# Kernel optimization log

Measured on AMD Instinct MI355X. Metric: run time of the kernel, lower is better.

## Reference

```python
import jax, jax.numpy as jnp
import numpy as np

N_NODES = 100000
N_EDGES = 3200000
N_GRAPHS = 512
D_IN = 128
N_CLASSES = 10
BN_EPS = 1e-5


def gcn_conv(x, W, b, src, dst, n_nodes):
    """PyG GCNConv: symmetric-normalized mean aggregation with self-loops."""
    h = x @ W  # [N, F_out]
    ones = jnp.ones(src.shape[0], h.dtype)
    deg = jax.ops.segment_sum(ones, dst, num_segments=n_nodes) + 1.0  # +1 self-loop
    dinv = jax.lax.rsqrt(deg)
    norm = dinv[src] * dinv[dst]  # [E]
    agg = jax.ops.segment_sum(h[src] * norm[:, None], dst, num_segments=n_nodes)
    agg = agg + h * (dinv * dinv)[:, None]  # self-loop contribution
    return agg + b


def bn_relu_lin(x, W, b, gamma, beta):
    """One MLP block: Linear -> ReLU -> BatchNorm1d (training-mode stats)."""
    h = jax.nn.relu(x @ W + b)
    m = h.mean(axis=0)
    v = h.var(axis=0)  # biased, like torch BN
    return gamma * (h - m) * jax.lax.rsqrt(v + BN_EPS) + beta


def setup_inputs() -> dict:
    key = jax.random.key(0)
    ks = jax.random.split(key, 16)
    x = jax.random.normal(ks[0], (N_NODES, D_IN), dtype=jnp.float32)
    edge_index = jax.random.randint(ks[1], (2, N_EDGES), 0, N_NODES, dtype=jnp.int64)
    batch = jnp.sort(jax.random.randint(ks[2], (N_NODES,), 0, N_GRAPHS, dtype=jnp.int64))

    def lin(k, fi, fo):
        s = 1.0 / np.sqrt(fi)
        kw, kb = jax.random.split(k)
        return (jax.random.uniform(kw, (fi, fo), jnp.float32, -s, s),
                jax.random.uniform(kb, (fo,), jnp.float32, -s, s))

    W1, b1 = lin(ks[3], D_IN, 32)
    W2, b2 = lin(ks[4], 32, 64)
    lin1_W, lin1_b = lin(ks[5], 96, 96)
    m1_W, m1_b = lin(ks[6], 96, 96)
    m2_W, m2_b = lin(ks[7], 96, N_CLASSES)
    return dict(
        x=x, edge_index=edge_index, batch=batch,
        W1=W1, b1=b1, W2=W2, b2=b2,
        lin1_W=lin1_W, lin1_b=lin1_b,
        lin1_g=jnp.ones((96,), jnp.float32), lin1_bt=jnp.zeros((96,), jnp.float32),
        m1_W=m1_W, m1_b=m1_b,
        m1_g=jnp.ones((96,), jnp.float32), m1_bt=jnp.zeros((96,), jnp.float32),
        m2_W=m2_W, m2_b=m2_b,
        m2_g=jnp.ones((N_CLASSES,), jnp.float32), m2_bt=jnp.zeros((N_CLASSES,), jnp.float32),
    )


def reference(x, edge_index, batch, W1, b1, W2, b2, lin1_W, lin1_b, lin1_g, lin1_bt,
              m1_W, m1_b, m1_g, m1_bt, m2_W, m2_b, m2_g, m2_bt):
    src, dst = edge_index[0], edge_index[1]
    x1 = gcn_conv(x, W1, b1, src, dst, N_NODES)   # [N, 32]
    x2 = gcn_conv(x1, W2, b2, src, dst, N_NODES)  # [N, 64]
    h = jnp.concatenate([x1, x2], axis=1)          # [N, 96]
    h = bn_relu_lin(h, lin1_W, lin1_b, lin1_g, lin1_bt)
    # global max pool over graphs
    pooled = jax.ops.segment_max(h, batch, num_segments=N_GRAPHS)
    pooled = jnp.where(jnp.isfinite(pooled), pooled, 0.0)  # guard empty segments
    h = bn_relu_lin(pooled, m1_W, m1_b, m1_g, m1_bt)
    out = bn_relu_lin(h, m2_W, m2_b, m2_g, m2_bt)  # [G, C]
    return out
```

## Files before the change

### kernel.cpp

```cpp
#include <hip/hip_runtime.h>
#include <hip/hip_fp16.h>

#define NN 100000
#define NE 3200000
#define NG 512
#define DIN 128
#define F1 32
#define F2 64
#define FC 96
#define NC 10
#define BNEPS 1e-5f

#define BSH 8
#define NBUK 391
#define EPB 16384
#define NBLK 196
#define SCAN_N (NBUK * NBLK)
#define SCAN_NB ((SCAN_N + 1023) / 1024)

typedef unsigned int uint;

__device__ __forceinline__ void atomAddF(float* p, float v) { unsafeAtomicAdd(p, v); }
__device__ __forceinline__ float2 h2f(uint u) {
  __half2 h = *reinterpret_cast<__half2*>(&u);
  return __half22float2(h);
}
__device__ __forceinline__ uint f2h2(float a, float b) {
  __half2 h = __floats2half2_rn(a, b);
  return *reinterpret_cast<uint*>(&h);
}

__global__ __launch_bounds__(256) void k_hist(const int* __restrict__ dst,
                                              unsigned* __restrict__ bhist) {
  __shared__ unsigned h[NBUK];
  int t = threadIdx.x, b = blockIdx.x;
  for (int i = t; i < NBUK; i += 256) h[i] = 0;
  __syncthreads();
  int beg = b * EPB, end = min(beg + EPB, NE);
  for (int e = beg + t; e < end; e += 256) atomicAdd(&h[dst[e] >> BSH], 1u);
  __syncthreads();
  for (int i = t; i < NBUK; i += 256) bhist[(size_t)i * NBLK + b] = h[i];
}

__global__ __launch_bounds__(256) void k_scan1(unsigned* __restrict__ data, int n,
                                               unsigned* __restrict__ bsum) {
  __shared__ unsigned ts[256];
  int b = blockIdx.x, t = threadIdx.x;
  int base = b * 1024 + t * 4;
  unsigned v0 = 0, v1 = 0, v2 = 0, v3 = 0;
  if (base + 3 < n) {
    uint4 u = *(const uint4*)&data[base];
    v0 = u.x; v1 = u.y; v2 = u.z; v3 = u.w;
  } else {
    if (base < n) v0 = data[base];
    if (base + 1 < n) v1 = data[base + 1];
    if (base + 2 < n) v2 = data[base + 2];
    if (base + 3 < n) v3 = data[base + 3];
  }
  unsigned s = v0 + v1 + v2 + v3;
  ts[t] = s;
  __syncthreads();
  for (int d = 1; d < 256; d <<= 1) {
    unsigned add = (t >= d) ? ts[t - d] : 0u;
    __syncthreads();
    ts[t] += add;
    __syncthreads();
  }
  unsigned run = ts[t] - s;
  if (t == 255) bsum[b] = ts[255];
  if (base < n) data[base] = run;
  run += v0;
  if (base + 1 < n) data[base + 1] = run;
  run += v1;
  if (base + 2 < n) data[base + 2] = run;
  run += v2;
  if (base + 3 < n) data[base + 3] = run;
}

__global__ void k_scan2(unsigned* __restrict__ bsum, int nb) {
  __shared__ unsigned ts[512];
  int t = threadIdx.x;
  unsigned v = (t < nb) ? bsum[t] : 0u;
  ts[t] = v;
  __syncthreads();
  for (int d = 1; d < 512; d <<= 1) {
    unsigned a = (t >= d) ? ts[t - d] : 0u;
    __syncthreads();
    ts[t] += a;
    __syncthreads();
  }
  if (t < nb) bsum[t] = ts[t] - v;
}

__global__ void k_scan3(unsigned* __restrict__ data, int n, const unsigned* __restrict__ bsum,
                        int total) {
  int i = blockIdx.x * 256 + threadIdx.x;
  if (i < n) data[i] += bsum[i >> 10];
  if (i == 0) data[n] = (unsigned)total;
}

__global__ __launch_bounds__(256) void k_binwrite(const int* __restrict__ src,
                                                  const int* __restrict__ dst,
                                                  const unsigned* __restrict__ offs2,
                                                  int* __restrict__ packed) {
  __shared__ unsigned cur[NBUK];
  int t = threadIdx.x, b = blockIdx.x;
  for (int i = t; i < NBUK; i += 256) cur[i] = offs2[(size_t)i * NBLK + b];
  __syncthreads();
  int beg = b * EPB, end = min(beg + EPB, NE);
  for (int e = beg + t; e < end; e += 256) {
    int d = dst[e];
    unsigned pos = atomicAdd(&cur[d >> BSH], 1u);
    packed[pos] = (src[e] << BSH) | (d & 255);
  }
}

__global__ __launch_bounds__(256) void k_bsort(const int* __restrict__ packed,
                                               const unsigned* __restrict__ offs2,
                                               int* __restrict__ csr,
                                               int* __restrict__ offs,
                                               float* __restrict__ dinv) {
  int buk = blockIdx.x, t = threadIdx.x;
  __shared__ unsigned cnt[256];
  __shared__ int cur[256];
  __shared__ unsigned wsum[4];
  cnt[t] = 0;
  __syncthreads();
  unsigned beg = offs2[(size_t)buk * NBLK], end = offs2[(size_t)(buk + 1) * NBLK];
  for (unsigned j = beg + t; j < end; j += 256) atomicAdd(&cnt[packed[j] & 255], 1u);
  __syncthreads();
  unsigned v = cnt[t];
  unsigned inc = v;
#pragma unroll
  for (int d = 1; d < 64; d <<= 1) {
    unsigned o = __shfl_up(inc, d, 64);
    if ((t & 63) >= d) inc += o;
  }
  int wv = t >> 6;
  if ((t & 63) == 63) wsum[wv] = inc;
  __syncthreads();
  unsigned woff = 0;
  for (int i = 0; i < wv; ++i) woff += wsum[i];
  unsigned ex = woff + inc - v;
  cur[t] = (int)(beg + ex);
  int node = (buk << BSH) + t;
  if (node < NN) {
    offs[node] = (int)(beg + ex);
    dinv[node] = rsqrtf((float)v + 1.0f);
  } else if (node == NN) {
    offs[NN] = (int)(beg + ex);
  }
  __syncthreads();
  for (unsigned j = beg + t; j < end; j += 256) {
    int p = packed[j];
    int pos = atomicAdd(&cur[p & 255], 1);
    csr[pos] = p >> BSH;
  }
}

__global__ void k_gbound(const int* __restrict__ batch, int* __restrict__ gstart) {
  int i = blockIdx.x * 256 + threadIdx.x;
  if (i >= NN) return;
  int b = batch[i], p = i ? batch[i - 1] : -1;
  for (int g = p + 1; g <= b; ++g) gstart[g] = i;
  if (i == NN - 1)
    for (int g = b + 1; g <= NG; ++g) gstart[g] = NN;
}

__global__ __launch_bounds__(256) void k_gemm1(const float* __restrict__ x,
                                               const float* __restrict__ W,
                                               const float* __restrict__ dinv,
                                               __half* __restrict__ h1sh) {
  __shared__ __align__(16) float Ws[DIN * F1];
  __shared__ __align__(16) float xs[64][DIN + 4];
  int t = threadIdx.x;
  for (int i = t; i < DIN * F1 / 4; i += 256)
    *(float4*)&Ws[i * 4] = *(const float4*)&W[i * 4];
  int row0 = blockIdx.x * 64;
  for (int i = t; i < 64 * 32; i += 256) {
    int r = i >> 5, q = i & 31;
    int row = row0 + r;
    float4 v = (row < NN) ? *(const float4*)&x[(size_t)row * DIN + q * 4]
                          : make_float4(0.f, 0.f, 0.f, 0.f);
    *(float4*)&xs[r][q * 4] = v;
  }
  __syncthreads();
  int cg = t & 7, rg = t >> 3;
  int c0 = cg * 4, r0 = rg * 2;
  float acc[2][4];
#pragma unroll
  for (int i = 0; i < 2; ++i)
#pragma unroll
    for (int j = 0; j < 4; ++j) acc[i][j] = 0.f;
#pragma unroll 4
  for (int k = 0; k < DIN; k += 4) {
    float4 xv0 = *(float4*)&xs[r0][k];
    float4 xv1 = *(float4*)&xs[r0 + 1][k];
    float4 wf[4];
#pragma unroll
    for (int m = 0; m < 4; ++m) wf[m] = *(float4*)&Ws[(k + m) * F1 + c0];
    const float* x0 = (const float*)&xv0;
    const float* x1 = (const float*)&xv1;
#pragma unroll
    for (int m = 0; m < 4; ++m) {
      const float* wp = (const float*)&wf[m];
#pragma unroll
      for (int j = 0; j < 4; ++j) {
        acc[0][j] += x0[m] * wp[j];
        acc[1][j] += x1[m] * wp[j];
      }
    }
  }
#pragma unroll
  for (int i = 0; i < 2; ++i) {
    int row = row0 + r0 + i;
    if (row < NN) {
      float dv = dinv[row];
      uint2 o;
      o.x = f2h2(acc[i][0] * dv, acc[i][1] * dv);
      o.y = f2h2(acc[i][2] * dv, acc[i][3] * dv);
      *(uint2*)&h1sh[(size_t)row * F1 + c0] = o;
    }
  }
}

__global__ __launch_bounds__(256) void k_gather1(const ushort* __restrict__ hs,
                                                 const int* __restrict__ offs,
                                                 const int* __restrict__ csr,
                                                 const float* __restrict__ dinv,
                                                 const float* __restrict__ bias,
                                                 float* __restrict__ out1,
                                                 uint* __restrict__ out2) {
  int node = blockIdx.x * 4 + (threadIdx.x >> 6);
  int lane = threadIdx.x & 63;
  int slot = lane >> 3, f4 = (lane & 7) * 4;
  int beg = offs[node], end = offs[node + 1];
  float ax = 0.f, ay = 0.f, az = 0.f, aw = 0.f;
  int j = beg + slot;
  for (; j + 8 < end; j += 16) {
    int s0 = csr[j], s1 = csr[j + 8];
    uint2 u0 = *(const uint2*)&hs[(size_t)s0 * F1 + f4];
    uint2 u1 = *(const uint2*)&hs[(size_t)s1 * F1 + f4];
    float2 a0 = h2f(u0.x), b0 = h2f(u0.y), a1 = h2f(u1.x), b1 = h2f(u1.y);
    ax += a0.x + a1.x; ay += a0.y + a1.y;
    az += b0.x + b1.x; aw += b0.y + b1.y;
  }
  if (j < end) {
    int s0 = csr[j];
    uint2 u0 = *(const uint2*)&hs[(size_t)s0 * F1 + f4];
    float2 a0 = h2f(u0.x), b0 = h2f(u0.y);
    ax += a0.x; ay += a0.y; az += b0.x; aw += b0.y;
  }
#pragma unroll
  for (int m = 8; m < 64; m <<= 1) {
    ax += __shfl_xor(ax, m, 64); ay += __shfl_xor(ay, m, 64);
    az += __shfl_xor(az, m, 64); aw += __shfl_xor(aw, m, 64);
  }
  if (slot == 0) {
    float dv = dinv[node];
    uint2 su = *(const uint2*)&hs[(size_t)node * F1 + f4];
    float2 sa = h2f(su.x), sb = h2f(su.y);
    float4 bb = *(const float4*)&bias[f4];
    float vx = dv * (sa.x + ax) + bb.x;
    float vy = dv * (sa.y + ay) + bb.y;
    float vz = dv * (sb.x + az) + bb.z;
    float vw = dv * (sb.y + aw) + bb.w;
    *(float4*)&out1[(size_t)node * FC + f4] = make_float4(vx, vy, vz, vw);
    uint2 o;
    o.x = f2h2(vx * dv, vy * dv);
    o.y = f2h2(vz * dv, vw * dv);
    *(uint2*)&out2[(size_t)node * 16 + (f4 >> 1)] = o;
  }
}

__global__ __launch_bounds__(256) void k_gather2f(const ushort* __restrict__ hs,
                                                  const int* __restrict__ offs,
                                                  const int* __restrict__ csr,
                                                  const float* __restrict__ dinv,
                                                  const float* __restrict__ W2,
                                                  const float* __restrict__ b2,
                                                  float* __restrict__ hcat) {
  __shared__ float rowbuf[4][F1];
  int wv = threadIdx.x >> 6;
  int node = blockIdx.x * 4 + wv;
  int lane = threadIdx.x & 63;
  int slot = lane >> 3, f4 = (lane & 7) * 4;
  int beg = offs[node], end = offs[node + 1];
  float ax = 0.f, ay = 0.f, az = 0.f, aw = 0.f;
  int j = beg + slot;
  for (; j + 8 < end; j += 16) {
    int s0 = csr[j], s1 = csr[j + 8];
    uint2 u0 = *(const uint2*)&hs[(size_t)s0 * F1 + f4];
    uint2 u1 = *(const uint2*)&hs[(size_t)s1 * F1 + f4];
    float2 a0 = h2f(u0.x), b0 = h2f(u0.y), a1 = h2f(u1.x), b1 = h2f(u1.y);
    ax += a0.x + a1.x; ay += a0.y + a1.y;
    az += b0.x + b1.x; aw += b0.y + b1.y;
  }
  if (j < end) {
    int s0 = csr[j];
    uint2 u0 = *(const uint2*)&hs[(size_t)s0 * F1 + f4];
    float2 a0 = h2f(u0.x), b0 = h2f(u0.y);
    ax += a0.x; ay += a0.y; az += b0.x; aw += b0.y;
  }
#pragma unroll
  for (int m = 8; m < 64; m <<= 1) {
    ax += __shfl_xor(ax, m, 64); ay += __shfl_xor(ay, m, 64);
    az += __shfl_xor(az, m, 64); aw += __shfl_xor(aw, m, 64);
  }
  if (slot == 0) {
    float dv = dinv[node];
    uint2 su = *(const uint2*)&hs[(size_t)node * F1 + f4];
    float2 sa = h2f(su.x), sb = h2f(su.y);
    *(float4*)&rowbuf[wv][f4] = make_float4(
        dv * (sa.x + ax), dv * (sa.y + ay),
        dv * (sb.x + az), dv * (sb.y + aw));
  }
  __syncthreads();
  const float* row = rowbuf[wv];
  float acc = b2[lane];
#pragma unroll
  for (int k = 0; k < F1; ++k) acc += row[k] * W2[k * F2 + lane];
  hcat[(size_t)node * FC + F1 + lane] = acc;
}

__global__ __launch_bounds__(384) void k_lin1(const float* __restrict__ hcat,
                                              const float* __restrict__ W,
                                              const float* __restrict__ b,
                                              float* __restrict__ y,
                                              float* __restrict__ colsum,
                                              float* __restrict__ colsumsq) {
  __shared__ __align__(16) float lds[16000];
  float* sW = lds;
  float* sX = lds + 9600;
  int t = threadIdx.x;
  for (int i = t; i < 96 * 24; i += 384) {
    int k = i / 24, c0 = (i % 24) * 4;
    float4 v = *(const float4*)&W[i * 4];
    *(float4*)&sW[k * 100 + c0] = v;
  }
  int row0 = blockIdx.x * 64;
  for (int i = t; i < 64 * 24; i += 384) {
    int r = i / 24, q = (i % 24) * 4;
    int row = row0 + r;
    float4 v = (row < NN) ? *(const float4*)&hcat[(size_t)row * FC + q]
                          : make_float4(0.f, 0.f, 0.f, 0.f);
    *(float4*)&sX[r * 100 + q] = v;
  }
  __syncthreads();
  int tx = t % 24, ty = t / 24;
  int c0 = tx * 4, r0 = ty * 4;
  float acc[4][4];
#pragma unroll
  for (int i = 0; i < 4; ++i)
#pragma unroll
    for (int j = 0; j < 4; ++j) acc[i][j] = 0.f;
#pragma unroll 4
  for (int k0 = 0; k0 < 96; k0 += 4) {
    float4 xf[4], wf[4];
#pragma unroll
    for (int i = 0; i < 4; ++i) xf[i] = *(float4*)&sX[(r0 + i) * 100 + k0];
#pragma unroll
    for (int m = 0; m < 4; ++m) wf[m] = *(float4*)&sW[(k0 + m) * 100 + c0];
#pragma unroll
    for (int i = 0; i < 4; ++i) {
      const float* xp = (const float*)&xf[i];
#pragma unroll
      for (int m = 0; m < 4; ++m) {
        const float* wp = (const float*)&wf[m];
#pragma unroll
        for (int j = 0; j < 4; ++j) acc[i][j] += xp[m] * wp[j];
      }
    }
  }
  float4 bb = *(const float4*)&b[c0];
  const float* bp = (const float*)&bb;
  float colp[4] = {0.f, 0.f, 0.f, 0.f}, colq[4] = {0.f, 0.f, 0.f, 0.f};
#pragma unroll
  for (int i = 0; i < 4; ++i) {
    int row = row0 + r0 + i;
    if (row < NN) {
      float v0 = fmaxf(acc[i][0] + bp[0], 0.f);
      float v1 = fmaxf(acc[i][1] + bp[1], 0.f);
      float v2 = fmaxf(acc[i][2] + bp[2], 0.f);
      float v3 = fmaxf(acc[i][3] + bp[3], 0.f);
      *(float4*)&y[(size_t)row * FC + c0] = make_float4(v0, v1, v2, v3);
      colp[0] += v0; colp[1] += v1; colp[2] += v2; colp[3] += v3;
      colq[0] += v0 * v0; colq[1] += v1 * v1; colq[2] += v2 * v2; colq[3] += v3 * v3;
    }
  }
  __syncthreads();
  float* ps = sX;
  float* pq = sX + 1536;
  *(float4*)&ps[ty * 96 + c0] = make_float4(colp[0], colp[1], colp[2], colp[3]);
  *(float4*)&pq[ty * 96 + c0] = make_float4(colq[0], colq[1], colq[2], colq[3]);
  __syncthreads();
  if (t < 96) {
    float s = 0.f, s2 = 0.f;
#pragma unroll
    for (int i = 0; i < 16; ++i) { s += ps[i * 96 + t]; s2 += pq[i * 96 + t]; }
    atomAddF(&colsum[t], s);
    atomAddF(&colsumsq[t], s2);
  }
}

__global__ __launch_bounds__(768) void k_pool(const float* __restrict__ y,
                                              const int* __restrict__ gstart,
                                              float* __restrict__ pooled) {
  int g = blockIdx.x, t = threadIdx.x;
  int c = t % FC, h = t / FC;
  int beg = gstart[g], end = gstart[g + 1];
  float m0 = 0.f, m1 = 0.f;
  int r = beg + h;
  for (; r + 8 < end; r += 16) {
    m0 = fmaxf(m0, y[(size_t)r * FC + c]);
    m1 = fmaxf(m1, y[(size_t)(r + 8) * FC + c]);
  }
  if (r < end) m0 = fmaxf(m0, y[(size_t)r * FC + c]);
  m0 = fmaxf(m0, m1);
  __shared__ float sh[8][FC];
  sh[h][c] = m0;
  __syncthreads();
  if (h == 0) {
    float m = sh[0][c];
#pragma unroll
    for (int i = 1; i < 8; ++i) m = fmaxf(m, sh[i][c]);
    pooled[(size_t)g * FC + c] = (end > beg) ? m : 0.f;
  }
}

__global__ void k_poolbn(const float* __restrict__ pooled, const float* __restrict__ colsum,
                         const float* __restrict__ colsumsq, const int* __restrict__ gstart,
                         const float* __restrict__ g1, const float* __restrict__ bt1,
                         float* __restrict__ pbn) {
  int idx = blockIdx.x * 256 + threadIdx.x;
  if (idx < NG * FC) {
    int g = idx / FC, c = idx % FC;
    float m = colsum[c] * (1.f / NN);
    float var = colsumsq[c] * (1.f / NN) - m * m;
    float rs = rsqrtf(var + BNEPS);
    float v = (gstart[g + 1] > gstart[g]) ? (g1[c] * (pooled[idx] - m) * rs + bt1[c]) : 0.f;
    pbn[idx] = v;
  }
}

__global__ __launch_bounds__(256) void k_mlp(const float* __restrict__ X, int ncol,
                                             const float* __restrict__ W,
                                             const float* __restrict__ b,
                                             const float* __restrict__ g,
                                             const float* __restrict__ bt,
                                             float* __restrict__ out) {
  int c = blockIdx.x, t = threadIdx.x;
  __shared__ float vals[NG];
  __shared__ float red[256], redq[256];
  __shared__ float wc[FC];
  if (t < FC) wc[t] = W[(size_t)t * ncol + c];
  __syncthreads();
  float psum = 0.f, psq = 0.f;
  for (int r = t; r < NG; r += 256) {
    float acc = b[c];
#pragma unroll
    for (int k = 0; k < FC; ++k) acc += X[(size_t)r * FC + k] * wc[k];
    float v = fmaxf(acc, 0.f);
    vals[r] = v;
    psum += v;
    psq += v * v;
  }
  red[t] = psum;
  redq[t] = psq;
  __syncthreads();
  for (int s = 128; s > 0; s >>= 1) {
    if (t < s) { red[t] += red[t + s]; redq[t] += redq[t + s]; }
    __syncthreads();
  }
  float m = red[0] * (1.f / NG);
  float var = redq[0] * (1.f / NG) - m * m;
  float rs = rsqrtf(var + BNEPS);
  float gg = g[c], bb = bt[c];
  for (int r = t; r < NG; r += 256) out[(size_t)r * ncol + c] = gg * (vals[r] - m) * rs + bb;
}

extern "C" void kernel_launch(void* const* d_in, const int* in_sizes, int n_in,
                              void* d_out, int out_size, void* d_ws, size_t ws_size,
                              hipStream_t stream) {
  const float* x    = (const float*)d_in[0];
  const int* ei     = (const int*)d_in[1];
  const int* src    = ei;
  const int* dst    = ei + NE;
  const int* batch  = (const int*)d_in[2];
  const float* W1   = (const float*)d_in[3];
  const float* b1   = (const float*)d_in[4];
  const float* W2   = (const float*)d_in[5];
  const float* b2   = (const float*)d_in[6];
  const float* l1W  = (const float*)d_in[7];
  const float* l1b  = (const float*)d_in[8];
  const float* l1g  = (const float*)d_in[9];
  const float* l1bt = (const float*)d_in[10];
  const float* m1W  = (const float*)d_in[11];
  const float* m1b  = (const float*)d_in[12];
  const float* m1g  = (const float*)d_in[13];
  const float* m1bt = (const float*)d_in[14];
  const float* m2W  = (const float*)d_in[15];
  const float* m2b  = (const float*)d_in[16];
  const float* m2g  = (const float*)d_in[17];
  const float* m2bt = (const float*)d_in[18];
  float* out = (float*)d_out;

  float* ws = (float*)d_ws;
  const size_t o_csum   = 0;
  const size_t o_csq    = 128;
  const size_t o_dinv   = 256;
  const size_t o_gstart = 100608;
  const size_t o_offs   = 101128;
  const size_t o_offs2  = 201488;
  const size_t o_bsum   = 507840;
  const size_t o_packed = 508144;
  const size_t o_h1sh   = 3708144;
  const size_t o_x1sh   = 5308144;
  const size_t o_csr    = 6908144;
  const size_t o_hcat   = 10108144;

  float* csum     = ws + o_csum;
  float* csq      = ws + o_csq;
  float* dinv     = ws + o_dinv;
  int* gstart     = (int*)(ws + o_gstart);
  int* offs       = (int*)(ws + o_offs);
  unsigned* offs2 = (unsigned*)(ws + o_offs2);
  unsigned* bsum  = (unsigned*)(ws + o_bsum);
  int* packed     = (int*)(ws + o_packed);
  __half* h1sh    = (__half*)(ws + o_h1sh);
  uint* x1sh      = (uint*)(ws + o_x1sh);
  int* csr        = (int*)(ws + o_csr);
  float* hcat     = ws + o_hcat;
  float* y        = ws + o_packed;
  float* pooled   = ws + o_offs2;
  float* pbn      = ws + o_offs2 + 49152;
  float* h3       = ws + o_offs2 + 98304;

  hipMemsetAsync(ws, 0, 256 * sizeof(float), stream);

  k_hist<<<NBLK, 256, 0, stream>>>(dst, offs2);
  k_scan1<<<SCAN_NB, 256, 0, stream>>>(offs2, SCAN_N, bsum);
  k_scan2<<<1, 512, 0, stream>>>(bsum, SCAN_NB);
  k_scan3<<<(SCAN_N + 255) / 256, 256, 0, stream>>>(offs2, SCAN_N, bsum, NE);
  k_binwrite<<<NBLK, 256, 0, stream>>>(src, dst, offs2, packed);
  k_bsort<<<NBUK, 256, 0, stream>>>(packed, offs2, csr, offs, dinv);
  k_gbound<<<(NN + 255) / 256, 256, 0, stream>>>(batch, gstart);

  k_gemm1<<<(NN + 63) / 64, 256, 0, stream>>>(x, W1, dinv, h1sh);
  k_gather1<<<NN / 4, 256, 0, stream>>>((const ushort*)h1sh, offs, csr, dinv, b1, hcat, x1sh);
  k_gather2f<<<NN / 4, 256, 0, stream>>>((const ushort*)x1sh, offs, csr, dinv, W2, b2, hcat);

  k_lin1<<<(NN + 63) / 64, 384, 0, stream>>>(hcat, l1W, l1b, y, csum, csq);
  k_pool<<<NG, 768, 0, stream>>>(y, gstart, pooled);
  k_poolbn<<<(NG * FC + 255) / 256, 256, 0, stream>>>(pooled, csum, csq, gstart, l1g, l1bt, pbn);

  k_mlp<<<FC, 256, 0, stream>>>(pbn, FC, m1W, m1b, m1g, m1bt, h3);
  k_mlp<<<NC, 256, 0, stream>>>(h3, NC, m2W, m2b, m2g, m2bt, out);
}
```

Measured before the change: 339.8 us.

## Split fp16 feature tables into 16-column halves for cache-resident gathers

Splits the 32-wide fp16 node feature tables into two 16-column arrays and runs each gather pass over one half, so each random-access table is half the size and more likely to stay in L2/MALL. The first-layer aggregation becomes two passes, and the second becomes a half-pass into a temp buffer plus a fused pass that combines both halves before the 32x64 projection. This adds two extra passes over the CSR indices and extra launches in exchange for better locality on the gathered feature rows.

```diff
diff --git a/kernel.cpp b/kernel.cpp
--- a/kernel.cpp
+++ b/kernel.cpp
@@ -170,7 +170,8 @@
 __global__ __launch_bounds__(256) void k_gemm1(const float* __restrict__ x,
                                                const float* __restrict__ W,
                                                const float* __restrict__ dinv,
-                                               __half* __restrict__ h1sh) {
+                                               ushort* __restrict__ h1a,
+                                               ushort* __restrict__ h1b) {
   __shared__ __align__(16) float Ws[DIN * F1];
   __shared__ __align__(16) float xs[64][DIN + 4];
   int t = threadIdx.x;
@@ -211,6 +212,8 @@
       }
     }
   }
+  ushort* dst = (c0 < 16) ? h1a : h1b;
+  int cc = c0 & 15;
 #pragma unroll
   for (int i = 0; i < 2; ++i) {
     int row = row0 + r0 + i;
@@ -219,61 +222,66 @@
       uint2 o;
       o.x = f2h2(acc[i][0] * dv, acc[i][1] * dv);
       o.y = f2h2(acc[i][2] * dv, acc[i][3] * dv);
-      *(uint2*)&h1sh[(size_t)row * F1 + c0] = o;
+      *(uint2*)&dst[(size_t)row * 16 + cc] = o;
     }
   }
 }
 
-__global__ __launch_bounds__(256) void k_gather1(const ushort* __restrict__ hs,
-                                                 const int* __restrict__ offs,
-                                                 const int* __restrict__ csr,
-                                                 const float* __restrict__ dinv,
-                                                 const float* __restrict__ bias,
-                                                 float* __restrict__ out1,
-                                                 uint* __restrict__ out2) {
+__global__ __launch_bounds__(256) void k_ghalf(const ushort* __restrict__ hs,
+                                               const int* __restrict__ offs,
+                                               const int* __restrict__ csr,
+                                               const float* __restrict__ dinv,
+                                               const float* __restrict__ bias,
+                                               float* __restrict__ out1,
+                                               uint* __restrict__ out2, int scale2) {
   int node = blockIdx.x * 4 + (threadIdx.x >> 6);
   int lane = threadIdx.x & 63;
-  int slot = lane >> 3, f4 = (lane & 7) * 4;
+  int slot = lane >> 2, fq = (lane & 3) * 4;
   int beg = offs[node], end = offs[node + 1];
   float ax = 0.f, ay = 0.f, az = 0.f, aw = 0.f;
   int j = beg + slot;
-  for (; j + 8 < end; j += 16) {
-    int s0 = csr[j], s1 = csr[j + 8];
-    uint2 u0 = *(const uint2*)&hs[(size_t)s0 * F1 + f4];
-    uint2 u1 = *(const uint2*)&hs[(size_t)s1 * F1 + f4];
+  for (; j + 16 < end; j += 32) {
+    int s0 = csr[j], s1 = csr[j + 16];
+    uint2 u0 = *(const uint2*)&hs[(size_t)s0 * 16 + fq];
+    uint2 u1 = *(const uint2*)&hs[(size_t)s1 * 16 + fq];
     float2 a0 = h2f(u0.x), b0 = h2f(u0.y), a1 = h2f(u1.x), b1 = h2f(u1.y);
     ax += a0.x + a1.x; ay += a0.y + a1.y;
     az += b0.x + b1.x; aw += b0.y + b1.y;
   }
   if (j < end) {
     int s0 = csr[j];
-    uint2 u0 = *(const uint2*)&hs[(size_t)s0 * F1 + f4];
+    uint2 u0 = *(const uint2*)&hs[(size_t)s0 * 16 + fq];
     float2 a0 = h2f(u0.x), b0 = h2f(u0.y);
     ax += a0.x; ay += a0.y; az += b0.x; aw += b0.y;
   }
 #pragma unroll
-  for (int m = 8; m < 64; m <<= 1) {
+  for (int m = 4; m < 64; m <<= 1) {
     ax += __shfl_xor(ax, m, 64); ay += __shfl_xor(ay, m, 64);
     az += __shfl_xor(az, m, 64); aw += __shfl_xor(aw, m, 64);
   }
   if (slot == 0) {
     float dv = dinv[node];
-    uint2 su = *(const uint2*)&hs[(size_t)node * F1 + f4];
+    uint2 su = *(const uint2*)&hs[(size_t)node * 16 + fq];
     float2 sa = h2f(su.x), sb = h2f(su.y);
-    float4 bb = *(const float4*)&bias[f4];
-    float vx = dv * (sa.x + ax) + bb.x;
-    float vy = dv * (sa.y + ay) + bb.y;
-    float vz = dv * (sb.x + az) + bb.z;
-    float vw = dv * (sb.y + aw) + bb.w;
-    *(float4*)&out1[(size_t)node * FC + f4] = make_float4(vx, vy, vz, vw);
-    uint2 o;
-    o.x = f2h2(vx * dv, vy * dv);
-    o.y = f2h2(vz * dv, vw * dv);
-    *(uint2*)&out2[(size_t)node * 16 + (f4 >> 1)] = o;
-  }
-}
-
-__global__ __launch_bounds__(256) void k_gather2f(const ushort* __restrict__ hs,
+    float vx = dv * (sa.x + ax), vy = dv * (sa.y + ay);
+    float vz = dv * (sb.x + az), vw = dv * (sb.y + aw);
+    if (bias) {
+      float4 bb = *(const float4*)&bias[fq];
+      vx += bb.x; vy += bb.y; vz += bb.z; vw += bb.w;
+    }
+    if (out1) *(float4*)&out1[(size_t)node * FC + fq] = make_float4(vx, vy, vz, vw);
+    if (out2) {
+      float s = scale2 ? dv : 1.f;
+      uint2 o;
+      o.x = f2h2(vx * s, vy * s);
+      o.y = f2h2(vz * s, vw * s);
+      *(uint2*)&out2[(size_t)node * 8 + (fq >> 1)] = o;
+    }
+  }
+}
+
+__global__ __launch_bounds__(256) void k_gather2b(const ushort* __restrict__ hs,
+                                                  const ushort* __restrict__ tmplo,
                                                   const int* __restrict__ offs,
                                                   const int* __restrict__ csr,
                                                   const float* __restrict__ dinv,
@@ -284,36 +292,43 @@
   int wv = threadIdx.x >> 6;
   int node = blockIdx.x * 4 + wv;
   int lane = threadIdx.x & 63;
-  int slot = lane >> 3, f4 = (lane & 7) * 4;
+  int slot = lane >> 2, fq = (lane & 3) * 4;
   int beg = offs[node], end = offs[node + 1];
   float ax = 0.f, ay = 0.f, az = 0.f, aw = 0.f;
   int j = beg + slot;
-  for (; j + 8 < end; j += 16) {
-    int s0 = csr[j], s1 = csr[j + 8];
-    uint2 u0 = *(const uint2*)&hs[(size_t)s0 * F1 + f4];
-    uint2 u1 = *(const uint2*)&hs[(size_t)s1 * F1 + f4];
+  for (; j + 16 < end; j += 32) {
+    int s0 = csr[j], s1 = csr[j + 16];
+    uint2 u0 = *(const uint2*)&hs[(size_t)s0 * 16 + fq];
+    uint2 u1 = *(const uint2*)&hs[(size_t)s1 * 16 + fq];
     float2 a0 = h2f(u0.x), b0 = h2f(u0.y), a1 = h2f(u1.x), b1 = h2f(u1.y);
     ax += a0.x + a1.x; ay += a0.y + a1.y;
     az += b0.x + b1.x; aw += b0.y + b1.y;
   }
   if (j < end) {
     int s0 = csr[j];
-    uint2 u0 = *(const uint2*)&hs[(size_t)s0 * F1 + f4];
+    uint2 u0 = *(const uint2*)&hs[(size_t)s0 * 16 + fq];
     float2 a0 = h2f(u0.x), b0 = h2f(u0.y);
     ax += a0.x; ay += a0.y; az += b0.x; aw += b0.y;
   }
 #pragma unroll
-  for (int m = 8; m < 64; m <<= 1) {
+  for (int m = 4; m < 64; m <<= 1) {
     ax += __shfl_xor(ax, m, 64); ay += __shfl_xor(ay, m, 64);
     az += __shfl_xor(az, m, 64); aw += __shfl_xor(aw, m, 64);
   }
   if (slot == 0) {
     float dv = dinv[node];
-    uint2 su = *(const uint2*)&hs[(size_t)node * F1 + f4];
+    uint2 su = *(const uint2*)&hs[(size_t)node * 16 + fq];
     float2 sa = h2f(su.x), sb = h2f(su.y);
-    *(float4*)&rowbuf[wv][f4] = make_float4(
-        dv * (sa.x + ax), dv * (sa.y + ay),
-        dv * (sb.x + az), dv * (sb.y + aw));
+    rowbuf[wv][16 + fq + 0] = dv * (sa.x + ax);
+    rowbuf[wv][16 + fq + 1] = dv * (sa.y + ay);
+    rowbuf[wv][16 + fq + 2] = dv * (sb.x + az);
+    rowbuf[wv][16 + fq + 3] = dv * (sb.y + aw);
+    uint2 tl = *(const uint2*)&tmplo[(size_t)node * 16 + fq];
+    float2 ta = h2f(tl.x), tb = h2f(tl.y);
+    rowbuf[wv][fq + 0] = ta.x;
+    rowbuf[wv][fq + 1] = ta.y;
+    rowbuf[wv][fq + 2] = tb.x;
+    rowbuf[wv][fq + 3] = tb.y;
   }
   __syncthreads();
   const float* row = rowbuf[wv];
@@ -514,8 +529,10 @@
   const size_t o_offs2  = 201488;
   const size_t o_bsum   = 507840;
   const size_t o_packed = 508144;
-  const size_t o_h1sh   = 3708144;
-  const size_t o_x1sh   = 5308144;
+  const size_t o_h1a    = 3708144;
+  const size_t o_h1b    = 4508144;
+  const size_t o_x1a    = 5308144;
+  const size_t o_x1b    = 6108144;
   const size_t o_csr    = 6908144;
   const size_t o_hcat   = 10108144;
 
@@ -527,8 +544,11 @@
   unsigned* offs2 = (unsigned*)(ws + o_offs2);
   unsigned* bsum  = (unsigned*)(ws + o_bsum);
   int* packed     = (int*)(ws + o_packed);
-  __half* h1sh    = (__half*)(ws + o_h1sh);
-  uint* x1sh      = (uint*)(ws + o_x1sh);
+  ushort* h1a     = (ushort*)(ws + o_h1a);
+  ushort* h1b     = (ushort*)(ws + o_h1b);
+  ushort* x1a     = (ushort*)(ws + o_x1a);
+  ushort* x1b     = (ushort*)(ws + o_x1b);
+  ushort* a2tmp   = (ushort*)(ws + o_h1a);
   int* csr        = (int*)(ws + o_csr);
   float* hcat     = ws + o_hcat;
   float* y        = ws + o_packed;
@@ -546,9 +566,12 @@
   k_bsort<<<NBUK, 256, 0, stream>>>(packed, offs2, csr, offs, dinv);
   k_gbound<<<(NN + 255) / 256, 256, 0, stream>>>(batch, gstart);
 
-  k_gemm1<<<(NN + 63) / 64, 256, 0, stream>>>(x, W1, dinv, h1sh);
-  k_gather1<<<NN / 4, 256, 0, stream>>>((const ushort*)h1sh, offs, csr, dinv, b1, hcat, x1sh);
-  k_gather2f<<<NN / 4, 256, 0, stream>>>((const ushort*)x1sh, offs, csr, dinv, W2, b2, hcat);
+  k_gemm1<<<(NN + 63) / 64, 256, 0, stream>>>(x, W1, dinv, h1a, h1b);
+  k_ghalf<<<NN / 4, 256, 0, stream>>>(h1a, offs, csr, dinv, b1, hcat, (uint*)x1a, 1);
+  k_ghalf<<<NN / 4, 256, 0, stream>>>(h1b, offs, csr, dinv, b1 + 16, hcat + 16, (uint*)x1b, 1);
+  k_ghalf<<<NN / 4, 256, 0, stream>>>(x1a, offs, csr, dinv, (const float*)nullptr,
+                                      (float*)nullptr, (uint*)a2tmp, 0);
+  k_gather2b<<<NN / 4, 256, 0, stream>>>(x1b, a2tmp, offs, csr, dinv, W2, b2, hcat);
 
   k_lin1<<<(NN + 63) / 64, 384, 0, stream>>>(hcat, l1W, l1b, y, csum, csq);
   k_pool<<<NG, 768, 0, stream>>>(y, gstart, pooled);
```

After: 396.8 us. +16.8%, slower.

## Fuse global max pooling into lin1 epilogue via integer atomicMax

Applied to the files above, without the earlier changes.

The separate pooling kernel, which re-read the full post-ReLU activation matrix, is removed. lin1 now stages each tile's ReLU outputs in shared memory and does a segmented max over the block's rows using per-row graph ids. Each segment is flushed with an integer atomicMax on the float bits, which is valid because the values are non-negative. This saves writing and re-reading a 100000x96 float intermediate and one launch, at the cost of a larger memset to zero the pooled buffer and a serial 64-row scan in 96 threads per block.

```diff
diff --git a/kernel.cpp b/kernel.cpp
--- a/kernel.cpp
+++ b/kernel.cpp
@@ -326,10 +326,12 @@
 __global__ __launch_bounds__(384) void k_lin1(const float* __restrict__ hcat,
                                               const float* __restrict__ W,
                                               const float* __restrict__ b,
-                                              float* __restrict__ y,
+                                              const int* __restrict__ batch,
+                                              float* __restrict__ pooled,
                                               float* __restrict__ colsum,
                                               float* __restrict__ colsumsq) {
   __shared__ __align__(16) float lds[16000];
+  __shared__ int bts[64];
   float* sW = lds;
   float* sX = lds + 9600;
   int t = threadIdx.x;
@@ -346,6 +348,7 @@
                           : make_float4(0.f, 0.f, 0.f, 0.f);
     *(float4*)&sX[r * 100 + q] = v;
   }
+  if (t < 64) bts[t] = (row0 + t < NN) ? batch[row0 + t] : -1;
   __syncthreads();
   int tx = t % 24, ty = t / 24;
   int c0 = tx * 4, r0 = ty * 4;
@@ -375,6 +378,7 @@
   float4 bb = *(const float4*)&b[c0];
   const float* bp = (const float*)&bb;
   float colp[4] = {0.f, 0.f, 0.f, 0.f}, colq[4] = {0.f, 0.f, 0.f, 0.f};
+  float yv[4][4];
 #pragma unroll
   for (int i = 0; i < 4; ++i) {
     int row = row0 + r0 + i;
@@ -383,14 +387,19 @@
       float v1 = fmaxf(acc[i][1] + bp[1], 0.f);
       float v2 = fmaxf(acc[i][2] + bp[2], 0.f);
       float v3 = fmaxf(acc[i][3] + bp[3], 0.f);
-      *(float4*)&y[(size_t)row * FC + c0] = make_float4(v0, v1, v2, v3);
+      yv[i][0] = v0; yv[i][1] = v1; yv[i][2] = v2; yv[i][3] = v3;
       colp[0] += v0; colp[1] += v1; colp[2] += v2; colp[3] += v3;
       colq[0] += v0 * v0; colq[1] += v1 * v1; colq[2] += v2 * v2; colq[3] += v3 * v3;
+    } else {
+      yv[i][0] = yv[i][1] = yv[i][2] = yv[i][3] = 0.f;
     }
   }
   __syncthreads();
-  float* ps = sX;
-  float* pq = sX + 1536;
+#pragma unroll
+  for (int i = 0; i < 4; ++i)
+    *(float4*)&sX[(r0 + i) * 100 + c0] = make_float4(yv[i][0], yv[i][1], yv[i][2], yv[i][3]);
+  float* ps = sW;
+  float* pq = sW + 1536;
   *(float4*)&ps[ty * 96 + c0] = make_float4(colp[0], colp[1], colp[2], colp[3]);
   *(float4*)&pq[ty * 96 + c0] = make_float4(colq[0], colq[1], colq[2], colq[3]);
   __syncthreads();
@@ -400,31 +409,18 @@
     for (int i = 0; i < 16; ++i) { s += ps[i * 96 + t]; s2 += pq[i * 96 + t]; }
     atomAddF(&colsum[t], s);
     atomAddF(&colsumsq[t], s2);
-  }
-}
-
-__global__ __launch_bounds__(768) void k_pool(const float* __restrict__ y,
-                                              const int* __restrict__ gstart,
-                                              float* __restrict__ pooled) {
-  int g = blockIdx.x, t = threadIdx.x;
-  int c = t % FC, h = t / FC;
-  int beg = gstart[g], end = gstart[g + 1];
-  float m0 = 0.f, m1 = 0.f;
-  int r = beg + h;
-  for (; r + 8 < end; r += 16) {
-    m0 = fmaxf(m0, y[(size_t)r * FC + c]);
-    m1 = fmaxf(m1, y[(size_t)(r + 8) * FC + c]);
-  }
-  if (r < end) m0 = fmaxf(m0, y[(size_t)r * FC + c]);
-  m0 = fmaxf(m0, m1);
-  __shared__ float sh[8][FC];
-  sh[h][c] = m0;
-  __syncthreads();
-  if (h == 0) {
-    float m = sh[0][c];
-#pragma unroll
-    for (int i = 1; i < 8; ++i) m = fmaxf(m, sh[i][c]);
-    pooled[(size_t)g * FC + c] = (end > beg) ? m : 0.f;
+    float runm = 0.f;
+    int curg = bts[0];
+    for (int r = 0; r < 64; ++r) {
+      int g = bts[r];
+      if (g != curg) {
+        if (curg >= 0) atomicMax((int*)&pooled[(size_t)curg * FC + t], __float_as_int(runm));
+        runm = 0.f;
+        curg = g;
+      }
+      if (g >= 0) runm = fmaxf(runm, sX[r * 100 + t]);
+    }
+    if (curg >= 0) atomicMax((int*)&pooled[(size_t)curg * FC + t], __float_as_int(runm));
   }
 }
 
@@ -508,19 +504,22 @@
   float* ws = (float*)d_ws;
   const size_t o_csum   = 0;
   const size_t o_csq    = 128;
-  const size_t o_dinv   = 256;
-  const size_t o_gstart = 100608;
-  const size_t o_offs   = 101128;
-  const size_t o_offs2  = 201488;
-  const size_t o_bsum   = 507840;
-  const size_t o_packed = 508144;
-  const size_t o_h1sh   = 3708144;
-  const size_t o_x1sh   = 5308144;
-  const size_t o_csr    = 6908144;
-  const size_t o_hcat   = 10108144;
+  const size_t o_pooled = 256;
+  const size_t o_zend   = 49408;
+  const size_t o_dinv   = 49408;
+  const size_t o_gstart = 149760;
+  const size_t o_offs   = 150280;
+  const size_t o_offs2  = 250640;
+  const size_t o_bsum   = 348944;
+  const size_t o_packed = 349248;
+  const size_t o_h1sh   = 3549248;
+  const size_t o_x1sh   = 5149248;
+  const size_t o_csr    = 6749248;
+  const size_t o_hcat   = 9949248;
 
   float* csum     = ws + o_csum;
   float* csq      = ws + o_csq;
+  float* pooled   = ws + o_pooled;
   float* dinv     = ws + o_dinv;
   int* gstart     = (int*)(ws + o_gstart);
   int* offs       = (int*)(ws + o_offs);
@@ -531,12 +530,10 @@
   uint* x1sh      = (uint*)(ws + o_x1sh);
   int* csr        = (int*)(ws + o_csr);
   float* hcat     = ws + o_hcat;
-  float* y        = ws + o_packed;
-  float* pooled   = ws + o_offs2;
-  float* pbn      = ws + o_offs2 + 49152;
-  float* h3       = ws + o_offs2 + 98304;
-
-  hipMemsetAsync(ws, 0, 256 * sizeof(float), stream);
+  float* pbn      = ws + o_offs2;
+  float* h3       = ws + o_offs2 + 49152;
+
+  hipMemsetAsync(ws, 0, o_zend * sizeof(float), stream);
 
   k_hist<<<NBLK, 256, 0, stream>>>(dst, offs2);
   k_scan1<<<SCAN_NB, 256, 0, stream>>>(offs2, SCAN_N, bsum);
@@ -550,8 +547,7 @@
   k_gather1<<<NN / 4, 256, 0, stream>>>((const ushort*)h1sh, offs, csr, dinv, b1, hcat, x1sh);
   k_gather2f<<<NN / 4, 256, 0, stream>>>((const ushort*)x1sh, offs, csr, dinv, W2, b2, hcat);
 
-  k_lin1<<<(NN + 63) / 64, 384, 0, stream>>>(hcat, l1W, l1b, y, csum, csq);
-  k_pool<<<NG, 768, 0, stream>>>(y, gstart, pooled);
+  k_lin1<<<(NN + 63) / 64, 384, 0, stream>>>(hcat, l1W, l1b, batch, pooled, csum, csq);
   k_poolbn<<<(NG * FC + 255) / 256, 256, 0, stream>>>(pooled, csum, csq, gstart, l1g, l1bt, pbn);
 
   k_mlp<<<FC, 256, 0, stream>>>(pbn, FC, m1W, m1b, m1g, m1bt, h3);
```

New measurement: 360.2 us. 1.06x slower.
